# Optimization experiments

Hardware: AMD Instinct MI355X
Metric: run time of the kernel (lower is better)

## Reference

```python
import jax, jax.numpy as jnp
import numpy as np

DIM = 128
HEADS = 8
C = DIM // HEADS  # per-head channel dim = 16
H = W = 256
B = 2


def setup_inputs() -> dict:
    key = jax.random.key(0)
    ks = jax.random.split(key, 6)
    x = jax.random.normal(ks[0], (B, DIM, H, W), jnp.float32)
    qkv_w = jax.random.normal(ks[1], (3 * DIM, DIM, 1, 1), jnp.float32) * 0.05
    dw_w = jax.random.normal(ks[2], (3 * DIM, 1, 3, 3), jnp.float32) * 0.05  # depthwise, groups=3*dim
    proj_w = jax.random.normal(ks[3], (DIM, DIM, 1, 1), jnp.float32) * 0.05
    attca_w = jax.random.normal(ks[4], (2 * C, C, 1, 1), jnp.float32) * 0.05
    temperature = jnp.ones((HEADS, 1, 1), jnp.float32)
    return {"x": x, "qkv_w": qkv_w, "dw_w": dw_w, "proj_w": proj_w,
            "attca_w": attca_w, "temperature": temperature}


def reference(x, qkv_w, dw_w, proj_w, attca_w, temperature):
    b, c_full, h, w = x.shape
    heads = temperature.shape[0]
    c = c_full // heads
    L = h * w

    # 1x1 conv qkv (pointwise -> einsum)
    qkv = jnp.einsum('bihw,oi->bohw', x, qkv_w[:, :, 0, 0])
    # 3x3 depthwise conv, groups = 3*dim
    qkv = jax.lax.conv_general_dilated(
        qkv, dw_w, window_strides=(1, 1), padding='SAME',
        dimension_numbers=('NCHW', 'OIHW', 'NCHW'),
        feature_group_count=3 * c_full)
    q, k, v = jnp.split(qkv, 3, axis=1)

    def to_heads(t):  # b (head c) h w -> b head c L
        return t.reshape(b, heads, c, L)
    q, k, v = to_heads(q), to_heads(k), to_heads(v)

    # F.normalize along last dim (eps=1e-12)
    q = q / jnp.maximum(jnp.linalg.norm(q, axis=-1, keepdims=True), 1e-12)
    k = k / jnp.maximum(jnp.linalg.norm(k, axis=-1, keepdims=True), 1e-12)

    # channel-wise attention scores: [b, head, c, c]
    attn = jnp.einsum('bhcl,bhdl->bhcd', q, k) * temperature

    attn0 = jax.nn.softmax(attn, axis=-1)
    a1 = jnp.square(jax.nn.relu(attn))
    a1 = jax.nn.gelu(a1, approximate=False) * a1

    # 'b head L c -> b c head L' then 1x1 conv over the (last) channel axis c
    a1p = jnp.transpose(a1, (0, 3, 1, 2))  # [b, c, head, c]
    xatt = jnp.einsum('bihd,oi->bohd', a1p, attca_w[:, :, 0, 0])  # [b, 2c, head, c]
    xatt = jnp.transpose(xatt, (0, 2, 3, 1))  # [b, head, c, 2c]
    scale, shift = jnp.split(xatt, 2, axis=-1)

    attn = attn0 * (1 + scale) + shift
    out = jnp.einsum('bhcd,bhdl->bhcl', attn, v).reshape(b, c_full, h, w)
    out = jnp.einsum('bihw,oi->bohw', out, proj_w[:, :, 0, 0])
    return out
```

## Files before the change

kernel.cpp:

```cpp
#include <hip/hip_runtime.h>
#include <hip/hip_bf16.h>
#include <math.h>

#define LL 65536
#define HH 256
#define WW 256
#define BB 2
#define DIMC 128
#define QKVC 384
#define NH 8
#define CH 16

typedef __hip_bfloat16 bf16;
typedef __attribute__((ext_vector_type(8))) __bf16 bf16x8;
typedef __attribute__((ext_vector_type(4))) float f32x4;
typedef __attribute__((ext_vector_type(4))) unsigned int u32x4;

static __device__ __forceinline__ float b2f(bf16 v){ return __bfloat162float(v); }
static __device__ __forceinline__ bf16  f2b(float v){ return __float2bfloat16(v); }
static __device__ __forceinline__ unsigned short fbits(float v){
  return __builtin_bit_cast(unsigned short, __float2bfloat16(v));
}

__global__ void k_wb(const float* __restrict__ w, unsigned short* __restrict__ wb){
  int idx = blockIdx.x*256 + threadIdx.x;
  if (idx < QKVC*DIMC) wb[idx] = fbits(w[idx]);
}

__global__ __launch_bounds__(512) void k_pw(const float* __restrict__ x,
                                            const unsigned short* __restrict__ wb,
                                            unsigned short* __restrict__ qkv){
  __shared__ u32x4 lds4[2048];
  char* lds = (char*)lds4;
  int bid = blockIdx.x;
  int b = bid >> 9;
  int l0 = (bid & 511) << 7;
  int tid = threadIdx.x;
  const float* xb = x + (size_t)b*DIMC*LL;

  #pragma unroll
  for (int it=0; it<4; ++it){
    int task = it*512 + tid;
    int l   = task & 127;
    int oct = task >> 7;
    float v[8];
    #pragma unroll
    for (int e=0;e<8;++e) v[e] = xb[(size_t)(oct*8+e)*LL + l0 + l];
    u32x4 p;
    #pragma unroll
    for (int k=0;k<4;++k){
      unsigned lo = fbits(v[2*k]);
      unsigned hi = fbits(v[2*k+1]);
      p[k] = lo | (hi<<16);
    }
    *(u32x4*)(lds + l*256 + ((oct ^ (l&15))<<4)) = p;
  }
  __syncthreads();

  int wid = tid >> 6, lane = tid & 63;
  int r = lane & 15, kg = lane >> 4;
  int ob = wid * 48;
  f32x4 acc[3][8];
  #pragma unroll
  for (int ft=0; ft<3; ++ft)
    #pragma unroll
    for (int nt=0; nt<8; ++nt) acc[ft][nt] = (f32x4)0.f;

  #pragma unroll
  for (int kb=0; kb<4; ++kb){
    bf16x8 a[3], bf[8];
    #pragma unroll
    for (int ft=0; ft<3; ++ft)
      a[ft] = *(const bf16x8*)(wb + (size_t)(ob + ft*16 + r)*DIMC + kb*32 + kg*8);
    #pragma unroll
    for (int nt=0; nt<8; ++nt){
      int l = nt*16 + r;
      bf[nt] = *(const bf16x8*)(lds + l*256 + (((kb*4 + kg) ^ r)<<4));
    }
    #pragma unroll
    for (int ft=0; ft<3; ++ft)
      #pragma unroll
      for (int nt=0; nt<8; ++nt)
        acc[ft][nt] = __builtin_amdgcn_mfma_f32_16x16x32_bf16(a[ft], bf[nt], acc[ft][nt], 0,0,0);
  }

  unsigned short* qb = qkv + (size_t)b*QKVC*LL + l0;
  #pragma unroll
  for (int ft=0; ft<3; ++ft)
    #pragma unroll
    for (int nt=0; nt<8; ++nt)
      #pragma unroll
      for (int i=0;i<4;++i){
        int o = ob + ft*16 + kg*4 + i;
        qb[(size_t)o*LL + nt*16 + r] = fbits(acc[ft][nt][i]);
      }
}

__global__ __launch_bounds__(256) void k_dw(const bf16* __restrict__ qkv,
                                            const float* __restrict__ dw,
                                            bf16* __restrict__ out){
  int bid = blockIdx.x;
  int rb = bid & 31;
  int ch = (bid >> 5) % QKVC;
  int b  = bid / (QKVC*32);
  int col = threadIdx.x;
  __shared__ float s[10][WW];
  const bf16* src = qkv + (size_t)(b*QKVC + ch)*LL;
  float wk[9];
  #pragma unroll
  for (int t=0;t<9;++t) wk[t] = dw[ch*9 + t];
  int r0 = rb*8;
  #pragma unroll
  for (int rr=0; rr<10; ++rr){
    int row = r0 - 1 + rr;
    s[rr][col] = (row >= 0 && row < HH) ? b2f(src[row*WW + col]) : 0.f;
  }
  __syncthreads();
  bf16* dst = out + (size_t)(b*QKVC + ch)*LL;
  #pragma unroll
  for (int r=0;r<8;++r){
    float acc = 0.f;
    #pragma unroll
    for (int dy=0;dy<3;++dy){
      float left  = (col>0)      ? s[r+dy][col-1] : 0.f;
      float mid   =                s[r+dy][col];
      float right = (col<WW-1)   ? s[r+dy][col+1] : 0.f;
      acc = fmaf(left,  wk[dy*3+0], acc);
      acc = fmaf(mid,   wk[dy*3+1], acc);
      acc = fmaf(right, wk[dy*3+2], acc);
    }
    dst[(r0+r)*WW + col] = f2b(acc);
  }
}

__global__ __launch_bounds__(256) void k_gram(const unsigned short* __restrict__ qkvd,
                                              float* __restrict__ S,
                                              float* __restrict__ nq,
                                              float* __restrict__ nk){
  int bid = blockIdx.x;
  int chunk = bid & 63;
  int h = (bid>>6)&7;
  int b = bid>>9;
  int tid = threadIdx.x, wid = tid>>6, lane = tid&63;
  int r = lane&15, kg = lane>>4;
  int l0 = chunk*1024 + wid*256;
  const unsigned short* qb = qkvd + (size_t)(b*QKVC + h*CH)*LL;
  const unsigned short* kb = qkvd + (size_t)(b*QKVC + DIMC + h*CH)*LL;
  f32x4 sqk = (f32x4)0.f, sqq = (f32x4)0.f, skk = (f32x4)0.f;
  #pragma unroll 4
  for (int ks=0; ks<8; ++ks){
    int l = l0 + ks*32 + kg*8;
    bf16x8 qf = *(const bf16x8*)(qb + (size_t)r*LL + l);
    bf16x8 kf = *(const bf16x8*)(kb + (size_t)r*LL + l);
    sqk = __builtin_amdgcn_mfma_f32_16x16x32_bf16(qf, kf, sqk, 0,0,0);
    sqq = __builtin_amdgcn_mfma_f32_16x16x32_bf16(qf, qf, sqq, 0,0,0);
    skk = __builtin_amdgcn_mfma_f32_16x16x32_bf16(kf, kf, skk, 0,0,0);
  }
  float* Sb = S + (size_t)((b*NH + h)*CH)*CH;
  #pragma unroll
  for (int i=0;i<4;++i)
    atomicAdd(&Sb[(kg*4+i)*CH + r], sqk[i]);
  if ((r>>2) == kg){
    int i = r&3;
    atomicAdd(&nq[(b*NH+h)*CH + r], sqq[i]);
    atomicAdd(&nk[(b*NH+h)*CH + r], skk[i]);
  }
}

__global__ __launch_bounds__(256) void k_fin(const float* __restrict__ S,
                                             const float* __restrict__ nq,
                                             const float* __restrict__ nk,
                                             const float* __restrict__ temp,
                                             const float* __restrict__ attca,
                                             const float* __restrict__ proj,
                                             unsigned short* __restrict__ M2){
  int b = blockIdx.x;
  int t = threadIdx.x;
  __shared__ float attnf[NH][CH][CH];
  __shared__ float pl[DIMC*DIMC];
  for (int idx=t; idx<DIMC*DIMC; idx+=256) pl[idx] = proj[idx];
  if (t < 128){
    int h = t >> 4, c = t & 15;
    float tmpv = temp[h];
    float qn = fmaxf(sqrtf(nq[(b*NH+h)*CH + c]), 1e-12f);
    float row[CH], ex[CH], a1[CH];
    float m = -1e30f;
    #pragma unroll
    for (int d=0; d<CH; ++d){
      float kn = fmaxf(sqrtf(nk[(b*NH+h)*CH + d]), 1e-12f);
      float v = S[((b*NH+h)*CH + c)*CH + d] / (qn*kn) * tmpv;
      row[d] = v;
      m = fmaxf(m, v);
    }
    float sum = 0.f;
    #pragma unroll
    for (int d=0;d<CH;++d){ ex[d] = expf(row[d]-m); sum += ex[d]; }
    float inv = 1.f/sum;
    #pragma unroll
    for (int d=0;d<CH;++d){
      float rr = fmaxf(row[d], 0.f);
      float xx = rr*rr;
      float g = 0.5f * xx * (1.f + erff(xx * 0.70710678118654752440f));
      a1[d] = g * xx;
    }
    #pragma unroll
    for (int j=0;j<CH;++j){
      float sc=0.f, sh=0.f;
      #pragma unroll
      for (int i=0;i<CH;++i){
        sc = fmaf(attca[j*CH+i],      a1[i], sc);
        sh = fmaf(attca[(CH+j)*CH+i], a1[i], sh);
      }
      attnf[h][c][j] = ex[j]*inv*(1.f+sc) + sh;
    }
  }
  __syncthreads();
  for (int idx=t; idx<DIMC*DIMC; idx+=256){
    int o = idx >> 7, j = idx & 127;
    int h = j >> 4, d = j & 15;
    float s = 0.f;
    #pragma unroll
    for (int c2=0;c2<CH;++c2) s = fmaf(pl[o*DIMC + h*CH + c2], attnf[h][c2][d], s);
    M2[(size_t)b*DIMC*DIMC + o*DIMC + j] = fbits(s);
  }
}

__global__ __launch_bounds__(256) void k_out(const unsigned short* __restrict__ qkvd,
                                             const unsigned short* __restrict__ M2,
                                             float* __restrict__ out){
  __shared__ u32x4 lds4[2048];
  char* lds = (char*)lds4;
  int bid = blockIdx.x;
  int b = bid >> 9;
  int l0 = (bid & 511) << 7;
  int tid = threadIdx.x;
  const unsigned short* vb = qkvd + (size_t)(b*QKVC + 2*DIMC)*LL;

  #pragma unroll
  for (int it=0; it<4; ++it){
    int task = it*256 + tid;
    int lp  = (task & 63) * 2;
    int oct = task >> 6;
    unsigned lo32[8];
    #pragma unroll
    for (int e=0;e<8;++e)
      lo32[e] = *(const unsigned int*)(vb + (size_t)(oct*8+e)*LL + l0 + lp);
    u32x4 p0, p1;
    #pragma unroll
    for (int k=0;k<4;++k){
      unsigned a0 = lo32[2*k] & 0xffffu,  a1 = lo32[2*k] >> 16;
      unsigned b0 = lo32[2*k+1] & 0xffffu, b1 = lo32[2*k+1] >> 16;
      p0[k] = a0 | (b0<<16);
      p1[k] = a1 | (b1<<16);
    }
    *(u32x4*)(lds + lp*256     + ((oct ^ (lp&15))<<4))     = p0;
    *(u32x4*)(lds + (lp+1)*256 + ((oct ^ ((lp+1)&15))<<4)) = p1;
  }
  __syncthreads();

  int wid = tid >> 6, lane = tid & 63;
  int r = lane & 15, kg = lane >> 4;
  int ob = wid * 32;
  f32x4 acc[2][8];
  #pragma unroll
  for (int ft=0; ft<2; ++ft)
    #pragma unroll
    for (int nt=0; nt<8; ++nt) acc[ft][nt] = (f32x4)0.f;

  #pragma unroll
  for (int kb=0; kb<4; ++kb){
    bf16x8 a[2], bf[8];
    #pragma unroll
    for (int ft=0; ft<2; ++ft)
      a[ft] = *(const bf16x8*)(M2 + (size_t)b*DIMC*DIMC + (ob + ft*16 + r)*DIMC + kb*32 + kg*8);
    #pragma unroll
    for (int nt=0; nt<8; ++nt){
      int l = nt*16 + r;
      bf[nt] = *(const bf16x8*)(lds + l*256 + (((kb*4 + kg) ^ r)<<4));
    }
    #pragma unroll
    for (int ft=0; ft<2; ++ft)
      #pragma unroll
      for (int nt=0; nt<8; ++nt)
        acc[ft][nt] = __builtin_amdgcn_mfma_f32_16x16x32_bf16(a[ft], bf[nt], acc[ft][nt], 0,0,0);
  }

  float* ob_ptr = out + (size_t)b*DIMC*LL + l0;
  #pragma unroll
  for (int ft=0; ft<2; ++ft)
    #pragma unroll
    for (int nt=0; nt<8; ++nt)
      #pragma unroll
      for (int i=0;i<4;++i){
        int o = ob + ft*16 + kg*4 + i;
        ob_ptr[(size_t)o*LL + nt*16 + r] = acc[ft][nt][i];
      }
}

extern "C" void kernel_launch(void* const* d_in, const int* in_sizes, int n_in,
                              void* d_out, int out_size, void* d_ws, size_t ws_size,
                              hipStream_t stream){
  const float* x      = (const float*)d_in[0];
  const float* qkv_w  = (const float*)d_in[1];
  const float* dw_w   = (const float*)d_in[2];
  const float* proj_w = (const float*)d_in[3];
  const float* attca  = (const float*)d_in[4];
  const float* temp   = (const float*)d_in[5];
  float* out = (float*)d_out;

  char* ws = (char*)d_ws;
  size_t off = 0;
  unsigned short* qkv_pw = (unsigned short*)(ws + off); off += (size_t)BB*QKVC*LL*2;
  unsigned short* qkv_dw = (unsigned short*)(ws + off); off += (size_t)BB*QKVC*LL*2;
  float* S  = (float*)(ws + off); off += (size_t)BB*NH*CH*CH*4;
  float* nq = (float*)(ws + off); off += (size_t)BB*NH*CH*4;
  float* nk = (float*)(ws + off); off += (size_t)BB*NH*CH*4;
  unsigned short* wb = (unsigned short*)(ws + off); off += (size_t)QKVC*DIMC*2;
  unsigned short* M2 = (unsigned short*)(ws + off); off += (size_t)BB*DIMC*DIMC*2;

  hipMemsetAsync(S, 0, (size_t)(BB*NH*CH*CH + 2*BB*NH*CH)*4, stream);

  k_wb  <<<(QKVC*DIMC + 255)/256, 256, 0, stream>>>(qkv_w, wb);
  k_pw  <<<BB*512,      512, 0, stream>>>(x, wb, qkv_pw);
  k_dw  <<<BB*QKVC*32,  256, 0, stream>>>((const bf16*)qkv_pw, dw_w, (bf16*)qkv_dw);
  k_gram<<<BB*512,      256, 0, stream>>>(qkv_dw, S, nq, nk);
  k_fin <<<BB,          256, 0, stream>>>(S, nq, nk, temp, attca, proj_w, M2);
  k_out <<<BB*512,      256, 0, stream>>>(qkv_dw, M2, out);
}
```

Measured before the change: 257.8 us.

## Fuse depthwise conv into Gram and output kernels; coalesce qkv stores via LDS

```diff
diff --git a/kernel.cpp b/kernel.cpp
--- a/kernel.cpp
+++ b/kernel.cpp
@@ -21,6 +21,9 @@
 static __device__ __forceinline__ unsigned short fbits(float v){
   return __builtin_bit_cast(unsigned short, __float2bfloat16(v));
 }
+static __device__ __forceinline__ float us2f(unsigned short u){
+  return __bfloat162float(__builtin_bit_cast(bf16, u));
+}
 
 __global__ void k_wb(const float* __restrict__ w, unsigned short* __restrict__ wb){
   int idx = blockIdx.x*256 + threadIdx.x;
@@ -32,6 +35,7 @@
                                             unsigned short* __restrict__ qkv){
   __shared__ u32x4 lds4[2048];
   char* lds = (char*)lds4;
+  unsigned short* lds16 = (unsigned short*)lds4;
   int bid = blockIdx.x;
   int b = bid >> 9;
   int l0 = (bid & 511) << 7;
@@ -85,76 +89,110 @@
   }
 
   unsigned short* qb = qkv + (size_t)b*QKVC*LL + l0;
-  #pragma unroll
-  for (int ft=0; ft<3; ++ft)
+  int gl = tid & 15;
+  int rowid = tid >> 4;
+  #pragma unroll
+  for (int ft=0; ft<3; ++ft){
+    __syncthreads();
     #pragma unroll
     for (int nt=0; nt<8; ++nt)
       #pragma unroll
       for (int i=0;i<4;++i){
-        int o = ob + ft*16 + kg*4 + i;
-        qb[(size_t)o*LL + nt*16 + r] = fbits(acc[ft][nt][i]);
-      }
-}
-
-__global__ __launch_bounds__(256) void k_dw(const bf16* __restrict__ qkv,
-                                            const float* __restrict__ dw,
-                                            bf16* __restrict__ out){
+        int o_l = wid*16 + kg*4 + i;
+        int l = nt*16 + r;
+        lds16[o_l*128 + (((l>>3) ^ ((o_l>>1)&7))<<3) + (l&7)] = fbits(acc[ft][nt][i]);
+      }
+    __syncthreads();
+    #pragma unroll
+    for (int j=0;j<4;++j){
+      int o_l = rowid*4 + j;
+      u32x4 v = *(u32x4*)(lds16 + o_l*128 + ((gl ^ ((o_l>>1)&7))<<3));
+      int o_g = (o_l>>4)*48 + ft*16 + (o_l&15);
+      *(u32x4*)(qb + (size_t)o_g*LL + gl*8) = v;
+    }
+  }
+}
+
+__global__ __launch_bounds__(512) void k_dwg(const unsigned short* __restrict__ qkvp,
+                                             const float* __restrict__ dww,
+                                             float* __restrict__ S,
+                                             float* __restrict__ nq,
+                                             float* __restrict__ nk){
+  __shared__ unsigned short q_l[16*1024];
+  __shared__ unsigned short k_l[16*1024];
   int bid = blockIdx.x;
-  int rb = bid & 31;
-  int ch = (bid >> 5) % QKVC;
-  int b  = bid / (QKVC*32);
-  int col = threadIdx.x;
-  __shared__ float s[10][WW];
-  const bf16* src = qkv + (size_t)(b*QKVC + ch)*LL;
-  float wk[9];
-  #pragma unroll
-  for (int t=0;t<9;++t) wk[t] = dw[ch*9 + t];
-  int r0 = rb*8;
-  #pragma unroll
-  for (int rr=0; rr<10; ++rr){
-    int row = r0 - 1 + rr;
-    s[rr][col] = (row >= 0 && row < HH) ? b2f(src[row*WW + col]) : 0.f;
-  }
-  __syncthreads();
-  bf16* dst = out + (size_t)(b*QKVC + ch)*LL;
-  #pragma unroll
-  for (int r=0;r<8;++r){
-    float acc = 0.f;
-    #pragma unroll
-    for (int dy=0;dy<3;++dy){
-      float left  = (col>0)      ? s[r+dy][col-1] : 0.f;
-      float mid   =                s[r+dy][col];
-      float right = (col<WW-1)   ? s[r+dy][col+1] : 0.f;
-      acc = fmaf(left,  wk[dy*3+0], acc);
-      acc = fmaf(mid,   wk[dy*3+1], acc);
-      acc = fmaf(right, wk[dy*3+2], acc);
-    }
-    dst[(r0+r)*WW + col] = f2b(acc);
-  }
-}
-
-__global__ __launch_bounds__(256) void k_gram(const unsigned short* __restrict__ qkvd,
-                                              float* __restrict__ S,
-                                              float* __restrict__ nq,
-                                              float* __restrict__ nk){
-  int bid = blockIdx.x;
-  int chunk = bid & 63;
-  int h = (bid>>6)&7;
-  int b = bid>>9;
-  int tid = threadIdx.x, wid = tid>>6, lane = tid&63;
-  int r = lane&15, kg = lane>>4;
-  int l0 = chunk*1024 + wid*256;
-  const unsigned short* qb = qkvd + (size_t)(b*QKVC + h*CH)*LL;
-  const unsigned short* kb = qkvd + (size_t)(b*QKVC + DIMC + h*CH)*LL;
+  int band = bid & 15;
+  int h    = (bid >> 4) & 7;
+  int b    = bid >> 7;
+  int tid  = threadIdx.x;
+  int col  = tid & 255;
+  int tch  = tid >> 8;
+  int lane = tid & 63;
+  int wid  = tid >> 6;
+  int r = lane & 15, kg = lane >> 4;
+
   f32x4 sqk = (f32x4)0.f, sqq = (f32x4)0.f, skk = (f32x4)0.f;
-  #pragma unroll 4
-  for (int ks=0; ks<8; ++ks){
-    int l = l0 + ks*32 + kg*8;
-    bf16x8 qf = *(const bf16x8*)(qb + (size_t)r*LL + l);
-    bf16x8 kf = *(const bf16x8*)(kb + (size_t)r*LL + l);
-    sqk = __builtin_amdgcn_mfma_f32_16x16x32_bf16(qf, kf, sqk, 0,0,0);
-    sqq = __builtin_amdgcn_mfma_f32_16x16x32_bf16(qf, qf, sqq, 0,0,0);
-    skk = __builtin_amdgcn_mfma_f32_16x16x32_bf16(kf, kf, skk, 0,0,0);
+
+  for (int sub=0; sub<4; ++sub){
+    int r0 = band*16 + sub*4;
+    for (int it=0; it<16; ++it){
+      int cc  = it*2 + tch;
+      int isk = cc >> 4;
+      int c   = cc & 15;
+      int och = isk*DIMC + h*CH + c;
+      const unsigned short* src = qkvp + ((size_t)b*QKVC + och)*LL;
+      const float* w9 = dww + och*9;
+      float w0=w9[0],w1=w9[1],w2=w9[2],w3=w9[3],w4=w9[4],w5=w9[5],w6=w9[6],w7=w9[7],w8=w9[8];
+      unsigned short* dst = (isk ? k_l : q_l) + c*1024;
+      float a0l,a0c,a0r,a1l,a1c,a1r;
+      {
+        int rr = r0-1;
+        float xc = (rr>=0) ? us2f(src[rr*WW + col]) : 0.f;
+        float xl = __shfl_up(xc,1);
+        float xr = __shfl_down(xc,1);
+        if (lane==0)  xl = (rr>=0 && col>0)    ? us2f(src[rr*WW + col-1]) : 0.f;
+        if (lane==63) xr = (rr>=0 && col<WW-1) ? us2f(src[rr*WW + col+1]) : 0.f;
+        a0l=xl; a0c=xc; a0r=xr;
+      }
+      {
+        int rr = r0;
+        float xc = us2f(src[rr*WW + col]);
+        float xl = __shfl_up(xc,1);
+        float xr = __shfl_down(xc,1);
+        if (lane==0)  xl = (col>0)    ? us2f(src[rr*WW + col-1]) : 0.f;
+        if (lane==63) xr = (col<WW-1) ? us2f(src[rr*WW + col+1]) : 0.f;
+        a1l=xl; a1c=xc; a1r=xr;
+      }
+      #pragma unroll
+      for (int rw=0; rw<4; ++rw){
+        int rr = r0 + rw + 1;
+        bool rok = (rr < HH);
+        float xc = rok ? us2f(src[rr*WW + col]) : 0.f;
+        float xl = __shfl_up(xc,1);
+        float xr = __shfl_down(xc,1);
+        if (lane==0)  xl = (rok && col>0)    ? us2f(src[rr*WW + col-1]) : 0.f;
+        if (lane==63) xr = (rok && col<WW-1) ? us2f(src[rr*WW + col+1]) : 0.f;
+        float acc;
+        acc = w0*a0l;               acc = fmaf(w1,a0c,acc); acc = fmaf(w2,a0r,acc);
+        acc = fmaf(w3,a1l,acc);     acc = fmaf(w4,a1c,acc); acc = fmaf(w5,a1r,acc);
+        acc = fmaf(w6,xl, acc);     acc = fmaf(w7,xc, acc); acc = fmaf(w8,xr, acc);
+        int px = rw*256 + col;
+        dst[(((px>>3) ^ c)<<3) + (px&7)] = fbits(acc);
+        a0l=a1l; a0c=a1c; a0r=a1r;
+        a1l=xl;  a1c=xc;  a1r=xr;
+      }
+    }
+    __syncthreads();
+    #pragma unroll
+    for (int kl=0; kl<4; ++kl){
+      int p = (wid*4 + kl)*4 + kg;
+      bf16x8 qf = *(const bf16x8*)(q_l + r*1024 + ((p ^ r)<<3));
+      bf16x8 kf = *(const bf16x8*)(k_l + r*1024 + ((p ^ r)<<3));
+      sqk = __builtin_amdgcn_mfma_f32_16x16x32_bf16(qf, kf, sqk, 0,0,0);
+      sqq = __builtin_amdgcn_mfma_f32_16x16x32_bf16(qf, qf, sqq, 0,0,0);
+      skk = __builtin_amdgcn_mfma_f32_16x16x32_bf16(kf, kf, skk, 0,0,0);
+    }
+    __syncthreads();
   }
   float* Sb = S + (size_t)((b*NH + h)*CH)*CH;
   #pragma unroll
@@ -225,40 +263,59 @@
   }
 }
 
-__global__ __launch_bounds__(256) void k_out(const unsigned short* __restrict__ qkvd,
+__global__ __launch_bounds__(256) void k_out(const unsigned short* __restrict__ qkvp,
+                                             const float* __restrict__ dww,
                                              const unsigned short* __restrict__ M2,
                                              float* __restrict__ out){
   __shared__ u32x4 lds4[2048];
   char* lds = (char*)lds4;
   int bid = blockIdx.x;
   int b = bid >> 9;
-  int l0 = (bid & 511) << 7;
+  int lt = bid & 511;
+  int row  = lt >> 1;
+  int col0 = (lt & 1) << 7;
+  int l0 = row*WW + col0;
   int tid = threadIdx.x;
-  const unsigned short* vb = qkvd + (size_t)(b*QKVC + 2*DIMC)*LL;
-
-  #pragma unroll
-  for (int it=0; it<4; ++it){
-    int task = it*256 + tid;
-    int lp  = (task & 63) * 2;
-    int oct = task >> 6;
-    unsigned lo32[8];
-    #pragma unroll
-    for (int e=0;e<8;++e)
-      lo32[e] = *(const unsigned int*)(vb + (size_t)(oct*8+e)*LL + l0 + lp);
-    u32x4 p0, p1;
-    #pragma unroll
-    for (int k=0;k<4;++k){
-      unsigned a0 = lo32[2*k] & 0xffffu,  a1 = lo32[2*k] >> 16;
-      unsigned b0 = lo32[2*k+1] & 0xffffu, b1 = lo32[2*k+1] >> 16;
-      p0[k] = a0 | (b0<<16);
-      p1[k] = a1 | (b1<<16);
-    }
-    *(u32x4*)(lds + lp*256     + ((oct ^ (lp&15))<<4))     = p0;
-    *(u32x4*)(lds + (lp+1)*256 + ((oct ^ ((lp+1)&15))<<4)) = p1;
+  int lane = tid & 63;
+  int p = tid & 127;
+  int gcol = col0 + p;
+  const unsigned short* vb = qkvp + ((size_t)b*QKVC + 2*DIMC)*LL;
+
+  #pragma unroll
+  for (int ii=0; ii<8; ++ii){
+    int oct = (tid>>7)*8 + ii;
+    u32x4 pk;
+    #pragma unroll
+    for (int e2=0; e2<4; ++e2){
+      unsigned lohi[2];
+      #pragma unroll
+      for (int hf=0; hf<2; ++hf){
+        int ch = oct*8 + e2*2 + hf;
+        const unsigned short* s = vb + (size_t)ch*LL;
+        const float* w9 = dww + (size_t)(2*DIMC + ch)*9;
+        float acc = 0.f;
+        #pragma unroll
+        for (int dy=-1; dy<=1; ++dy){
+          int rr = row + dy;
+          bool rok = (rr>=0 && rr<HH);
+          float xc = rok ? us2f(s[rr*WW + gcol]) : 0.f;
+          float xl = __shfl_up(xc,1);
+          float xr = __shfl_down(xc,1);
+          if (lane==0)  xl = (rok && gcol>0)    ? us2f(s[rr*WW + gcol-1]) : 0.f;
+          if (lane==63) xr = (rok && gcol<WW-1) ? us2f(s[rr*WW + gcol+1]) : 0.f;
+          acc = fmaf(xl, w9[(dy+1)*3+0], acc);
+          acc = fmaf(xc, w9[(dy+1)*3+1], acc);
+          acc = fmaf(xr, w9[(dy+1)*3+2], acc);
+        }
+        lohi[hf] = fbits(acc);
+      }
+      pk[e2] = lohi[0] | (lohi[1]<<16);
+    }
+    *(u32x4*)(lds + p*256 + ((oct ^ (p&15))<<4)) = pk;
   }
   __syncthreads();
 
-  int wid = tid >> 6, lane = tid & 63;
+  int wid = tid >> 6;
   int r = lane & 15, kg = lane >> 4;
   int ob = wid * 32;
   f32x4 acc[2][8];
@@ -311,7 +368,6 @@
   char* ws = (char*)d_ws;
   size_t off = 0;
   unsigned short* qkv_pw = (unsigned short*)(ws + off); off += (size_t)BB*QKVC*LL*2;
-  unsigned short* qkv_dw = (unsigned short*)(ws + off); off += (size_t)BB*QKVC*LL*2;
   float* S  = (float*)(ws + off); off += (size_t)BB*NH*CH*CH*4;
   float* nq = (float*)(ws + off); off += (size_t)BB*NH*CH*4;
   float* nk = (float*)(ws + off); off += (size_t)BB*NH*CH*4;
@@ -321,9 +377,8 @@
   hipMemsetAsync(S, 0, (size_t)(BB*NH*CH*CH + 2*BB*NH*CH)*4, stream);
 
   k_wb  <<<(QKVC*DIMC + 255)/256, 256, 0, stream>>>(qkv_w, wb);
-  k_pw  <<<BB*512,      512, 0, stream>>>(x, wb, qkv_pw);
-  k_dw  <<<BB*QKVC*32,  256, 0, stream>>>((const bf16*)qkv_pw, dw_w, (bf16*)qkv_dw);
-  k_gram<<<BB*512,      256, 0, stream>>>(qkv_dw, S, nq, nk);
-  k_fin <<<BB,          256, 0, stream>>>(S, nq, nk, temp, attca, proj_w, M2);
-  k_out <<<BB*512,      256, 0, stream>>>(qkv_dw, M2, out);
-}
+  k_pw  <<<BB*512,       512, 0, stream>>>(x, wb, qkv_pw);
+  k_dwg <<<BB*NH*16,     512, 0, stream>>>(qkv_pw, dw_w, S, nq, nk);
+  k_fin <<<BB,           256, 0, stream>>>(S, nq, nk, temp, attca, proj_w, M2);
+  k_out <<<BB*512,       256, 0, stream>>>(qkv_pw, dw_w, M2, out);
+}
```

New measurement: 711.8 us. +176.1%, slower.

## Stage pointwise-conv output through LDS for vector stores; vectorize depthwise conv

Applied to the files above, without the earlier changes.

```diff
diff --git a/kernel.cpp b/kernel.cpp
--- a/kernel.cpp
+++ b/kernel.cpp
@@ -17,9 +17,11 @@
 typedef __attribute__((ext_vector_type(4))) unsigned int u32x4;
 
 static __device__ __forceinline__ float b2f(bf16 v){ return __bfloat162float(v); }
-static __device__ __forceinline__ bf16  f2b(float v){ return __float2bfloat16(v); }
 static __device__ __forceinline__ unsigned short fbits(float v){
   return __builtin_bit_cast(unsigned short, __float2bfloat16(v));
+}
+static __device__ __forceinline__ float us2f(unsigned short u){
+  return __bfloat162float(__builtin_bit_cast(bf16, u));
 }
 
 __global__ void k_wb(const float* __restrict__ w, unsigned short* __restrict__ wb){
@@ -32,6 +34,7 @@
                                             unsigned short* __restrict__ qkv){
   __shared__ u32x4 lds4[2048];
   char* lds = (char*)lds4;
+  unsigned short* lds16 = (unsigned short*)lds4;
   int bid = blockIdx.x;
   int b = bid >> 9;
   int l0 = (bid & 511) << 7;
@@ -85,52 +88,93 @@
   }
 
   unsigned short* qb = qkv + (size_t)b*QKVC*LL + l0;
-  #pragma unroll
-  for (int ft=0; ft<3; ++ft)
+  int gl = tid & 15;
+  int rowid = tid >> 4;
+  #pragma unroll
+  for (int ft=0; ft<3; ++ft){
+    __syncthreads();
     #pragma unroll
     for (int nt=0; nt<8; ++nt)
       #pragma unroll
       for (int i=0;i<4;++i){
-        int o = ob + ft*16 + kg*4 + i;
-        qb[(size_t)o*LL + nt*16 + r] = fbits(acc[ft][nt][i]);
+        int o_l = wid*16 + kg*4 + i;
+        int l = nt*16 + r;
+        lds16[o_l*128 + (((l>>3) ^ ((o_l>>1)&7))<<3) + (l&7)] = fbits(acc[ft][nt][i]);
       }
-}
-
-__global__ __launch_bounds__(256) void k_dw(const bf16* __restrict__ qkv,
+    __syncthreads();
+    #pragma unroll
+    for (int j=0;j<4;++j){
+      int o_l = rowid*4 + j;
+      u32x4 v = *(u32x4*)(lds16 + o_l*128 + ((gl ^ ((o_l>>1)&7))<<3));
+      int o_g = (o_l>>4)*48 + ft*16 + (o_l&15);
+      *(u32x4*)(qb + (size_t)o_g*LL + gl*8) = v;
+    }
+  }
+}
+
+__global__ __launch_bounds__(256) void k_dw(const unsigned short* __restrict__ src_,
                                             const float* __restrict__ dw,
-                                            bf16* __restrict__ out){
+                                            unsigned short* __restrict__ dst_){
   int bid = blockIdx.x;
-  int rb = bid & 31;
+  int band = bid & 31;
   int ch = (bid >> 5) % QKVC;
   int b  = bid / (QKVC*32);
-  int col = threadIdx.x;
-  __shared__ float s[10][WW];
-  const bf16* src = qkv + (size_t)(b*QKVC + ch)*LL;
-  float wk[9];
-  #pragma unroll
-  for (int t=0;t<9;++t) wk[t] = dw[ch*9 + t];
-  int r0 = rb*8;
-  #pragma unroll
-  for (int rr=0; rr<10; ++rr){
-    int row = r0 - 1 + rr;
-    s[rr][col] = (row >= 0 && row < HH) ? b2f(src[row*WW + col]) : 0.f;
-  }
-  __syncthreads();
-  bf16* dst = out + (size_t)(b*QKVC + ch)*LL;
-  #pragma unroll
-  for (int r=0;r<8;++r){
-    float acc = 0.f;
-    #pragma unroll
-    for (int dy=0;dy<3;++dy){
-      float left  = (col>0)      ? s[r+dy][col-1] : 0.f;
-      float mid   =                s[r+dy][col];
-      float right = (col<WW-1)   ? s[r+dy][col+1] : 0.f;
-      acc = fmaf(left,  wk[dy*3+0], acc);
-      acc = fmaf(mid,   wk[dy*3+1], acc);
-      acc = fmaf(right, wk[dy*3+2], acc);
-    }
-    dst[(r0+r)*WW + col] = f2b(acc);
-  }
+  int t = threadIdx.x;
+  int rowl = t >> 5;
+  int seg  = t & 31;
+  int grow = band*8 + rowl;
+  const unsigned short* src = src_ + ((size_t)b*QKVC + ch)*LL;
+  const float* w9 = dw + ch*9;
+
+  float v[3][8];
+  #pragma unroll
+  for (int dy=0; dy<3; ++dy){
+    int rr = grow + dy - 1;
+    if (rr >= 0 && rr < HH){
+      u32x4 raw = *(const u32x4*)(src + (size_t)rr*WW + seg*8);
+      #pragma unroll
+      for (int k=0;k<4;++k){
+        v[dy][2*k]   = us2f((unsigned short)(raw[k] & 0xffffu));
+        v[dy][2*k+1] = us2f((unsigned short)(raw[k] >> 16));
+      }
+    } else {
+      #pragma unroll
+      for (int e=0;e<8;++e) v[dy][e] = 0.f;
+    }
+  }
+  int lane = t & 63;
+  float lft[3], rgt[3];
+  #pragma unroll
+  for (int dy=0; dy<3; ++dy){
+    float lv = __shfl(v[dy][7], lane-1);
+    float rv = __shfl(v[dy][0], lane+1);
+    lft[dy] = (seg==0)  ? 0.f : lv;
+    rgt[dy] = (seg==31) ? 0.f : rv;
+  }
+  float w0=w9[0],w1=w9[1],w2=w9[2],w3=w9[3],w4=w9[4],w5=w9[5],w6=w9[6],w7=w9[7],w8=w9[8];
+  float o[8];
+  #pragma unroll
+  for (int e=0;e<8;++e){
+    float l0 = (e==0) ? lft[0] : v[0][e-1];
+    float l1 = (e==0) ? lft[1] : v[1][e-1];
+    float l2 = (e==0) ? lft[2] : v[2][e-1];
+    float r0 = (e==7) ? rgt[0] : v[0][e+1];
+    float r1 = (e==7) ? rgt[1] : v[1][e+1];
+    float r2 = (e==7) ? rgt[2] : v[2][e+1];
+    float a;
+    a = w0*l0;            a = fmaf(w1, v[0][e], a); a = fmaf(w2, r0, a);
+    a = fmaf(w3, l1, a);  a = fmaf(w4, v[1][e], a); a = fmaf(w5, r1, a);
+    a = fmaf(w6, l2, a);  a = fmaf(w7, v[2][e], a); a = fmaf(w8, r2, a);
+    o[e] = a;
+  }
+  u32x4 pk;
+  #pragma unroll
+  for (int k=0;k<4;++k){
+    unsigned lo = fbits(o[2*k]);
+    unsigned hi = fbits(o[2*k+1]);
+    pk[k] = lo | (hi<<16);
+  }
+  *(u32x4*)(dst_ + ((size_t)b*QKVC + ch)*LL + (size_t)grow*WW + seg*8) = pk;
 }
 
 __global__ __launch_bounds__(256) void k_gram(const unsigned short* __restrict__ qkvd,
@@ -321,9 +365,9 @@
   hipMemsetAsync(S, 0, (size_t)(BB*NH*CH*CH + 2*BB*NH*CH)*4, stream);
 
   k_wb  <<<(QKVC*DIMC + 255)/256, 256, 0, stream>>>(qkv_w, wb);
-  k_pw  <<<BB*512,      512, 0, stream>>>(x, wb, qkv_pw);
-  k_dw  <<<BB*QKVC*32,  256, 0, stream>>>((const bf16*)qkv_pw, dw_w, (bf16*)qkv_dw);
-  k_gram<<<BB*512,      256, 0, stream>>>(qkv_dw, S, nq, nk);
-  k_fin <<<BB,          256, 0, stream>>>(S, nq, nk, temp, attca, proj_w, M2);
-  k_out <<<BB*512,      256, 0, stream>>>(qkv_dw, M2, out);
-}
+  k_pw  <<<BB*512,       512, 0, stream>>>(x, wb, qkv_pw);
+  k_dw  <<<BB*QKVC*32,   256, 0, stream>>>(qkv_pw, dw_w, qkv_dw);
+  k_gram<<<BB*512,       256, 0, stream>>>(qkv_dw, S, nq, nk);
+  k_fin <<<BB,           256, 0, stream>>>(S, nq, nk, temp, attca, proj_w, M2);
+  k_out <<<BB*512,       256, 0, stream>>>(qkv_dw, M2, out);
+}
```

After: 254.7 us. Within noise of the previous version (-1.2%).
